# Kernel tuning notes

Hardware: AMD Instinct MI355X
Metric: run time of the kernel (lower is better)

The kernel has to match this reference:

```python
import jax, jax.numpy as jnp
import numpy as np

VAR0, VAR1 = 0.1, 0.2       # variances used by encode()
THRESH = 0.35               # overlap_thresh
NEGPOS = 7                  # negpos_ratio


def point_form(p):
    # (cx,cy,w,h) -> (xmin,ymin,xmax,ymax)
    return jnp.concatenate([p[:, :2] - p[:, 2:] / 2, p[:, :2] + p[:, 2:] / 2], axis=1)


def jaccard(a, b):
    # a:[G,4], b:[P,4] corner form -> IoU [G,P]
    lt = jnp.maximum(a[:, None, :2], b[None, :, :2])
    rb = jnp.minimum(a[:, None, 2:], b[None, :, 2:])
    wh = jnp.clip(rb - lt, 0.0, None)
    inter = wh[..., 0] * wh[..., 1]
    area_a = (a[:, 2] - a[:, 0]) * (a[:, 3] - a[:, 1])
    area_b = (b[:, 2] - b[:, 0]) * (b[:, 3] - b[:, 1])
    return inter / (area_a[:, None] + area_b[None, :] - inter)


def encode(matched, priors):
    g_cxcy = ((matched[:, :2] + matched[:, 2:]) / 2 - priors[:, :2]) / (VAR0 * priors[:, 2:])
    g_wh = jnp.log((matched[:, 2:] - matched[:, :2]) / priors[:, 2:]) / VAR1
    return jnp.concatenate([g_cxcy, g_wh], axis=1)


def encode_landm(matched, priors):
    m = matched.reshape(-1, 5, 2)                                  # [P,5,2]
    g = (m - priors[:, None, :2]) / (VAR0 * priors[:, None, 2:])
    return g.reshape(-1, 10)


def match_one(truths, labels, landms, priors, priors_pf):
    # truths:[G,4] labels:[G] landms:[G,10] priors:[P,4](cxcywh) priors_pf:[P,4](corner)
    G = truths.shape[0]
    P = priors.shape[0]
    ov = jaccard(truths, priors_pf)                                # [G,P]
    best_prior_ov = ov.max(axis=1)                                 # [G]
    best_prior_idx = ov.argmax(axis=1)                             # [G]
    valid_gt = best_prior_ov >= 0.2
    best_truth_ov = ov.max(axis=0)                                 # [P]
    best_truth_idx = ov.argmax(axis=0)                             # [P]
    # index_fill_(0, best_prior_idx[valid_gt], 2): 2 > any IoU, so max is equivalent
    forced_ov = jnp.zeros((P,), ov.dtype).at[best_prior_idx].max(jnp.where(valid_gt, 2.0, 0.0))
    best_truth_ov = jnp.maximum(best_truth_ov, forced_ov)
    forced_idx = jnp.full((P,), -1, jnp.int32).at[best_prior_idx].max(jnp.arange(G, dtype=jnp.int32))
    best_truth_idx = jnp.where(forced_idx >= 0, forced_idx, best_truth_idx.astype(jnp.int32))
    conf = labels[best_truth_idx].astype(jnp.int32)
    conf = jnp.where(best_truth_ov < THRESH, 0, conf)
    loc = encode(truths[best_truth_idx], priors)                   # [P,4]
    landm = encode_landm(landms[best_truth_idx], priors)           # [P,10]
    # if no valid gt, torch zeroes the targets for this sample
    any_valid = valid_gt.any()
    loc = jnp.where(any_valid, loc, 0.0)
    landm = jnp.where(any_valid, landm, 0.0)
    conf = jnp.where(any_valid, conf, 0)
    return loc, conf, landm


def smooth_l1(x):
    ax = jnp.abs(x)
    return jnp.where(ax < 1.0, 0.5 * ax * ax, ax - 0.5)


def setup_inputs() -> dict:
    key = jax.random.key(0)
    k1, k2, k3, k4, k5, k6, k7, k8, k9 = jax.random.split(key, 9)
    B, P, G, C = 64, 16800, 32, 2
    cls_data = jax.random.normal(k1, (B, P, C), jnp.float32)
    loc_data = jax.random.normal(k2, (B, P, 4), jnp.float32)
    landm_data = jax.random.normal(k3, (B, P, 10), jnp.float32)
    # priors in (cx,cy,w,h), w,h in [0.02,0.3]
    pc = jax.random.uniform(k4, (P, 2), jnp.float32)
    pwh = jax.random.uniform(k5, (P, 2), jnp.float32, 0.02, 0.3)
    priors = jnp.concatenate([pc, pwh], axis=1)
    # targets: [B,G,15] = 4 box (corner form, valid) + 10 landmarks + 1 label
    c = jax.random.uniform(k6, (B, G, 2), jnp.float32, 0.15, 0.85)
    s = jax.random.uniform(k7, (B, G, 2), jnp.float32, 0.02, 0.3)
    boxes = jnp.concatenate([c - s / 2, c + s / 2], axis=-1)
    lms = jax.random.uniform(k8, (B, G, 10), jnp.float32)
    labels = jnp.where(jax.random.uniform(k9, (B, G, 1)) < 0.3, -1.0, 1.0)
    targets = jnp.concatenate([boxes, lms, labels], axis=-1)
    return {"cls_data": cls_data, "loc_data": loc_data, "landm_data": landm_data,
            "priors": priors, "targets": targets}


def reference(cls_data, loc_data, landm_data, priors, targets):
    truths = targets[:, :, :4]
    landms = targets[:, :, 4:14]
    labels = targets[:, :, 14]
    priors_pf = point_form(priors)
    loc_t, conf_t, landm_t = jax.vmap(
        lambda t, l, lm: match_one(t, l, lm, priors, priors_pf))(truths, labels, landms)
    num, P = conf_t.shape

    # landmark loss (smooth L1 over conf_t > 0)
    pos1 = conf_t > 0
    N1 = jnp.maximum(pos1.sum().astype(jnp.float32), 1.0)
    loss_landm = jnp.sum(smooth_l1(landm_data - landm_t) * pos1[..., None].astype(landm_data.dtype))

    # localization loss (smooth L1 over conf_t != 0)
    pos = conf_t != 0
    conf_t = jnp.where(pos, 1, conf_t)                              # conf_t[pos] = 1
    loss_l = jnp.sum(smooth_l1(loc_data - loc_t) * pos[..., None].astype(loc_data.dtype))

    # hard negative mining on per-prior CE loss
    logz = jax.nn.logsumexp(cls_data, axis=-1)                      # [B,P]
    gold = jnp.take_along_axis(cls_data, conf_t[..., None], axis=-1)[..., 0]
    loss_c = jnp.where(pos, 0.0, logz - gold)
    loss_idx = jnp.argsort(-loss_c, axis=1)
    idx_rank = jnp.argsort(loss_idx, axis=1)
    num_pos = pos.sum(axis=1, keepdims=True)
    num_neg = jnp.clip(NEGPOS * num_pos, None, P - 1)
    neg = idx_rank < num_neg

    sel = (pos | neg).astype(cls_data.dtype)
    loss_conf = jnp.sum((logz - gold) * sel)

    N = jnp.maximum(num_pos.sum().astype(jnp.float32), 1.0)
    return loss_l / N, loss_conf / N, loss_landm / N1
```

## Files before the change

### kernel.cpp

```cpp
#include <hip/hip_runtime.h>
#include <hip/hip_bf16.h>
#include <math.h>


#define RCP(x) __builtin_amdgcn_rcpf(x)

constexpr int GN = 32;

__device__ __forceinline__ float sl1(float x) {
    float a = fabsf(x);
    return a < 1.f ? 0.5f * a * a : a - 0.5f;
}

constexpr int GPB = 4;
constexpr int GNT = 512;
__global__ __launch_bounds__(GNT)
void k_gt(const float4* __restrict__ priors, const float* __restrict__ targets,
          unsigned long long* __restrict__ keys, int P, int G) {
    const int b = blockIdx.y, g0 = blockIdx.x * GPB, tid = threadIdx.x;
    const int lane = tid & 63, w = tid >> 6;
    __shared__ float4 s_box[GPB];
    __shared__ float  s_at[GPB];
    __shared__ unsigned long long s_wk[GNT / 64][GPB];
    if (tid < GPB) {
        const float* t = targets + ((size_t)b * G + g0 + tid) * 15;
        float4 v = make_float4(t[0], t[1], t[2], t[3]);
        s_box[tid] = v;
        s_at[tid] = (v.z - v.x) * (v.w - v.y);
    }
    __syncthreads();
    float4 tb0 = s_box[0], tb1 = s_box[1], tb2 = s_box[2], tb3 = s_box[3];
    float at0 = s_at[0], at1 = s_at[1], at2 = s_at[2], at3 = s_at[3];

    float bv[GPB]; int bp[GPB];
    #pragma unroll
    for (int j = 0; j < GPB; ++j) { bv[j] = -1.f; bp[j] = 0; }

    for (int p = tid; p < P; p += GNT) {
        float4 pr = priors[p];
        float hx = pr.z * 0.5f, hy = pr.w * 0.5f;
        float px0 = pr.x - hx, py0 = pr.y - hy;
        float px1 = pr.x + hx, py1 = pr.y + hy;
        float ap = (px1 - px0) * (py1 - py0);
        #pragma unroll
        for (int j = 0; j < GPB; ++j) {
            float4 tb = j == 0 ? tb0 : (j == 1 ? tb1 : (j == 2 ? tb2 : tb3));
            float at = j == 0 ? at0 : (j == 1 ? at1 : (j == 2 ? at2 : at3));
            float lx = fmaxf(tb.x, px0), ly = fmaxf(tb.y, py0);
            float rx = fminf(tb.z, px1), ry = fminf(tb.w, py1);
            float iw = fmaxf(rx - lx, 0.f), ih = fmaxf(ry - ly, 0.f);
            float inter = iw * ih;
            float iou = inter * RCP(at + ap - inter);
            if (iou > bv[j]) { bv[j] = iou; bp[j] = p; }
        }
    }
    #pragma unroll
    for (int j = 0; j < GPB; ++j) {
        unsigned long long key =
            ((unsigned long long)__float_as_uint(bv[j]) << 32) | ~(unsigned)bp[j];
        #pragma unroll
        for (int o = 32; o > 0; o >>= 1) {
            unsigned long long t = __shfl_down(key, o, 64);
            if (t > key) key = t;
        }
        if (lane == 0) s_wk[w][j] = key;
    }
    __syncthreads();
    if (tid < GPB) {
        unsigned long long m = 0ull;
        #pragma unroll
        for (int q = 0; q < GNT / 64; ++q) { unsigned long long t = s_wk[q][tid]; if (t > m) m = t; }
        keys[b * G + g0 + tid] = m;
    }
}

__global__ __launch_bounds__(256)
void k_match(const float2* __restrict__ cls, const float4* __restrict__ loc,
             const float* __restrict__ lmd, const float4* __restrict__ priors,
             const float* __restrict__ targets,
             const unsigned long long* __restrict__ keys,
             float* __restrict__ bc, float* __restrict__ part, int P, int NB) {
    const int b = blockIdx.y, bx = blockIdx.x, tid = threadIdx.x;
    const int lane = tid & 63, w = tid >> 6;
    __shared__ float4 s_box[GN];
    __shared__ float  s_at[GN];
    __shared__ float  s_c035[GN];
    __shared__ float  s_lm[GN * 10];
    __shared__ float  s_lab[GN];
    __shared__ int    s_fg[256];
    __shared__ int    s_fv[256];
    __shared__ unsigned s_vm;
    __shared__ float  s_red[4][8];

    s_fg[tid] = -1; s_fv[tid] = 0;
    for (int i = tid; i < GN * 15; i += 256) {
        int g = i / 15, j = i - g * 15;
        float v = targets[((size_t)b * GN + g) * 15 + j];
        if (j < 4) ((float*)&s_box[g])[j] = v;
        else if (j < 14) s_lm[g * 10 + (j - 4)] = v;
        else s_lab[g] = v;
    }
    __syncthreads();
    if (tid < GN) {
        float4 v = s_box[tid];
        float at = (v.z - v.x) * (v.w - v.y);
        s_at[tid] = at;
        s_c035[tid] = 0.35f * at;
        unsigned long long key = keys[b * GN + tid];
        unsigned bp = ~(unsigned)key;
        bool val = __uint_as_float((unsigned)(key >> 32)) >= 0.2f;
        unsigned long long bal = __ballot(val);
        if (tid == 0) s_vm = (unsigned)bal;
        int local = (int)bp - bx * 256;
        if (local >= 0 && local < 256) {
            atomicMax(&s_fg[local], tid);
            if (val) atomicOr(&s_fv[local], 1);
        }
    }
    __syncthreads();
    const bool av = s_vm != 0u;
    const int  fidx = s_fg[tid];
    const bool fv = s_fv[tid] != 0;

    int p = bx * 256 + tid;
    const bool act = p < P;
    float4 pr = act ? priors[p] : make_float4(0.f, 0.f, 0.f, 0.f);
    float hx = pr.z * 0.5f, hy = pr.w * 0.5f;
    float px0 = pr.x - hx, py0 = pr.y - hy;
    float px1 = pr.x + hx, py1 = pr.y + hy;
    float ap = (px1 - px0) * (py1 - py0);
    if (!act) { px0 = py0 = INFINITY; px1 = py1 = -INFINITY; }

    float wx0 = px0, wy0 = py0, wx1 = px1, wy1 = py1;
    #pragma unroll
    for (int o = 32; o > 0; o >>= 1) {
        wx0 = fminf(wx0, __shfl_xor(wx0, o, 64));
        wy0 = fminf(wy0, __shfl_xor(wy0, o, 64));
        wx1 = fmaxf(wx1, __shfl_xor(wx1, o, 64));
        wy1 = fmaxf(wy1, __shfl_xor(wy1, o, 64));
    }
    bool sg = false;
    if (lane < GN) {
        float4 tb = s_box[lane];
        sg = (tb.x < wx1) && (tb.z > wx0) && (tb.y < wy1) && (tb.w > wy0);
    }
    unsigned mask = (unsigned)__ballot(sg);

    float qmax = -INFINITY;
    unsigned m2 = mask;
    while (m2) {
        int g = __ffs(m2) - 1; m2 &= m2 - 1;
        float4 tb = s_box[g];
        float lx = fmaxf(tb.x, px0), ly = fmaxf(tb.y, py0);
        float rx = fminf(tb.z, px1), ry = fminf(tb.w, py1);
        float iw = fmaxf(rx - lx, 0.f), ih = fmaxf(ry - ly, 0.f);
        float inter = iw * ih;
        qmax = fmaxf(qmax, fmaf(1.35f, inter, -s_c035[g]));
    }
    bool thr = act && (qmax >= 0.35f * ap);
    bool pos = act && av && (fv || thr);

    float lse = 0.f, d = 0.f;
    if (act) {
        float2 c = cls[(size_t)b * P + p];
        d = c.y - c.x;
        float m0 = fmaxf(d, 0.f);
        lse = m0 + __logf(__expf(-m0) + __expf(d - m0));
        bc[(size_t)b * P + p] = pos ? 0.f : lse;
    }

    float a_ll = 0.f, a_lm = 0.f, a_lcp = 0.f;
    bool posl = false;
    if (pos) {
        a_lcp = lse - d;
        int bti2 = fidx;
        if (fidx < 0) {
            float btv = -1.f;
            unsigned m3 = mask;
            while (m3) {
                int g = __ffs(m3) - 1; m3 &= m3 - 1;
                float4 tb = s_box[g];
                float lx = fmaxf(tb.x, px0), ly = fmaxf(tb.y, py0);
                float rx = fminf(tb.z, px1), ry = fminf(tb.w, py1);
                float iw = fmaxf(rx - lx, 0.f), ih = fmaxf(ry - ly, 0.f);
                float inter = iw * ih;
                float iou = inter * RCP(s_at[g] + ap - inter);
                if (iou > btv) { btv = iou; bti2 = g; }
            }
        }
        float4 tb = s_box[bti2];
        float rw = RCP(pr.z), rh = RCP(pr.w);
        float e0 = ((tb.x + tb.z) * 0.5f - pr.x) * rw * 10.f;
        float e1 = ((tb.y + tb.w) * 0.5f - pr.y) * rh * 10.f;
        float e2 = __logf((tb.z - tb.x) * rw) * 5.f;
        float e3 = __logf((tb.w - tb.y) * rh) * 5.f;
        float4 ld = loc[(size_t)b * P + p];
        a_ll = sl1(ld.x - e0) + sl1(ld.y - e1) + sl1(ld.z - e2) + sl1(ld.w - e3);
        if (s_lab[bti2] > 0.f) {
            posl = true;
            const float* lp = lmd + ((size_t)b * P + p) * 10;
            #pragma unroll
            for (int q = 0; q < 5; ++q) {
                float gx = (s_lm[bti2 * 10 + 2 * q]     - pr.x) * rw * 10.f;
                float gy = (s_lm[bti2 * 10 + 2 * q + 1] - pr.y) * rh * 10.f;
                a_lm += sl1(lp[2 * q] - gx) + sl1(lp[2 * q + 1] - gy);
            }
        }
    }

    unsigned long long bpos = __ballot(pos);
    int npw  = __popcll(bpos);
    int np1w = __popcll(__ballot(posl));
    if (bpos) {
        #pragma unroll
        for (int o = 32; o > 0; o >>= 1) {
            a_ll  += __shfl_down(a_ll,  o, 64);
            a_lm  += __shfl_down(a_lm,  o, 64);
            a_lcp += __shfl_down(a_lcp, o, 64);
        }
    }
    if (lane == 0) {
        s_red[w][0] = a_ll; s_red[w][1] = a_lm; s_red[w][2] = a_lcp;
        s_red[w][3] = (float)npw; s_red[w][4] = (float)np1w;
    }
    __syncthreads();
    if (tid == 0) {
        float* pp = part + ((size_t)b * NB + bx) * 8;
        #pragma unroll
        for (int j = 0; j < 5; ++j)
            pp[j] = s_red[0][j] + s_red[1][j] + s_red[2][j] + s_red[3][j];
    }
}

constexpr int SNT = 1024;
constexpr int SNI = 17;
__global__ __launch_bounds__(SNT)
void k_select(const float* __restrict__ bc, const float* __restrict__ part,
              float* __restrict__ part2, int P, int NB) {
    const int b = blockIdx.x, tid = threadIdx.x;
    const int lane = tid & 63, w = tid >> 6;
    unsigned ul[SNI];
    #pragma unroll
    for (int i = 0; i < SNI; ++i) {
        int idx = i * SNT + tid;
        ul[i] = idx < P ? __float_as_uint(bc[(size_t)b * P + idx]) : 0u;
    }
    __shared__ float s_r[5];
    if (w < 5) {
        float s = 0.f;
        for (int bx = lane; bx < NB; bx += 64) s += part[((size_t)b * NB + bx) * 8 + w];
        #pragma unroll
        for (int o = 32; o > 0; o >>= 1) s += __shfl_down(s, o, 64);
        if (lane == 0) s_r[w] = s;
    }
    __syncthreads();
    float t_ll = s_r[0], t_lm = s_r[1], t_lcp = s_r[2], t_np = s_r[3], t_np1 = s_r[4];
    int np = (int)(t_np + 0.5f);
    int k = np * 7;
    if (k > P - 1) k = P - 1;

    __shared__ int s_ri[16];
    __shared__ int s_i0;
    __shared__ float s_rf[16];
    float topk = 0.f;
    if (k > 0) {
        unsigned lo = 0u, hi = 0x7f800000u;
        while (lo < hi) {
            unsigned mid = lo + ((hi - lo + 1) >> 1);
            int cnt = 0;
            #pragma unroll
            for (int i = 0; i < SNI; ++i) cnt += (ul[i] >= mid) ? 1 : 0;
            #pragma unroll
            for (int o = 32; o > 0; o >>= 1) cnt += __shfl_down(cnt, o, 64);
            if (lane == 0) s_ri[w] = cnt;
            __syncthreads();
            if (tid == 0) {
                int r = 0;
                #pragma unroll
                for (int q = 0; q < 16; ++q) r += s_ri[q];
                s_i0 = r;
            }
            __syncthreads();
            if (s_i0 >= k) lo = mid; else hi = mid - 1;
        }
        float fT = __uint_as_float(lo);
        float s = 0.f; int c = 0;
        #pragma unroll
        for (int i = 0; i < SNI; ++i)
            if (ul[i] > lo) { s += __uint_as_float(ul[i]); c++; }
        #pragma unroll
        for (int o = 32; o > 0; o >>= 1) {
            s += __shfl_down(s, o, 64);
            c += __shfl_down(c, o, 64);
        }
        if (lane == 0) { s_rf[w] = s; s_ri[w] = c; }
        __syncthreads();
        if (tid == 0) {
            float ts = 0.f; int tc = 0;
            #pragma unroll
            for (int q = 0; q < 16; ++q) { ts += s_rf[q]; tc += s_ri[q]; }
            topk = ts + (float)(k - tc) * fT;
        }
    }
    if (tid == 0) {
        float* pp = part2 + b * 8;
        pp[0] = t_ll; pp[1] = t_lm; pp[2] = t_lcp;
        pp[3] = topk; pp[4] = t_np; pp[5] = t_np1;
    }
}

__global__ void k_final(const float* __restrict__ part2, float* __restrict__ out, int B) {
    int lane = threadIdx.x;
    float ll = 0, lm = 0, lcp = 0, tk = 0, np = 0, np1 = 0;
    for (int b = lane; b < B; b += 64) {
        const float* pp = part2 + b * 8;
        ll += pp[0]; lm += pp[1]; lcp += pp[2];
        tk += pp[3]; np += pp[4]; np1 += pp[5];
    }
    #pragma unroll
    for (int o = 32; o > 0; o >>= 1) {
        ll  += __shfl_down(ll, o, 64);
        lm  += __shfl_down(lm, o, 64);
        lcp += __shfl_down(lcp, o, 64);
        tk  += __shfl_down(tk, o, 64);
        np  += __shfl_down(np, o, 64);
        np1 += __shfl_down(np1, o, 64);
    }
    if (lane == 0) {
        float N = fmaxf(np, 1.f), N1 = fmaxf(np1, 1.f);
        out[0] = ll / N;
        out[1] = (lcp + tk) / N;
        out[2] = lm / N1;
    }
}

extern "C" void kernel_launch(void* const* d_in, const int* in_sizes, int n_in,
                              void* d_out, int out_size, void* d_ws, size_t ws_size,
                              hipStream_t stream) {
    const float2* cls    = (const float2*)d_in[0];
    const float4* loc    = (const float4*)d_in[1];
    const float* lmd     = (const float*)d_in[2];
    const float4* priors = (const float4*)d_in[3];
    const float* targets = (const float*)d_in[4];
    int P = in_sizes[3] / 4;
    int B = (in_sizes[1] / 4) / P;
    int NB = (P + 255) / 256;
    int G = in_sizes[4] / (15 * B);

    size_t off = 0;
    unsigned long long* keys = (unsigned long long*)d_ws; off += (size_t)B * G * 8;
    float* part  = (float*)((char*)d_ws + off); off += (size_t)B * NB * 8 * 4;
    float* part2 = (float*)((char*)d_ws + off); off += (size_t)B * 8 * 4;
    off = (off + 255) & ~(size_t)255;
    float* bc = (float*)((char*)d_ws + off);

    dim3 ggt((G + GPB - 1) / GPB, B);
    k_gt<<<ggt, GNT, 0, stream>>>(priors, targets, keys, P, G);
    dim3 gm(NB, B);
    k_match<<<gm, 256, 0, stream>>>(cls, loc, lmd, priors, targets, keys, bc, part, P, NB);
    k_select<<<B, SNT, 0, stream>>>(bc, part, part2, P, NB);
    k_final<<<1, 64, 0, stream>>>(part2, (float*)d_out, B);
}
```

Before: 96.60 us.

## Restructure match/select: bitmask positives, fuse CE into select, 4-way search, fused final

k_match now handles 1024 priors per block (4 per thread) with a fixed unrolled GT loop instead of wave-culled masks, and writes a positive bitmask in place of per-prior loss values. The logsumexp and CE computation moves into k_select, which reads cls directly and derives positive counts and loss sums there. The threshold search now tests three split points per round (quaternary search) to cut the number of barrier rounds. k_final is folded into k_select through a last-block atomic counter, removing one launch. In exchange, k_select does more per-batch serial work with fewer threads, each holding more values in registers.

```diff
diff --git a/kernel.cpp b/kernel.cpp
--- a/kernel.cpp
+++ b/kernel.cpp
@@ -4,6 +4,7 @@
 
 
 #define RCP(x) __builtin_amdgcn_rcpf(x)
+typedef unsigned long long u64;
 
 constexpr int GN = 32;
 
@@ -16,12 +17,13 @@
 constexpr int GNT = 512;
 __global__ __launch_bounds__(GNT)
 void k_gt(const float4* __restrict__ priors, const float* __restrict__ targets,
-          unsigned long long* __restrict__ keys, int P, int G) {
+          u64* __restrict__ keys, int* __restrict__ done, int P, int G) {
     const int b = blockIdx.y, g0 = blockIdx.x * GPB, tid = threadIdx.x;
     const int lane = tid & 63, w = tid >> 6;
+    if (blockIdx.x == 0 && blockIdx.y == 0 && tid == 0) *done = 0;
     __shared__ float4 s_box[GPB];
     __shared__ float  s_at[GPB];
-    __shared__ unsigned long long s_wk[GNT / 64][GPB];
+    __shared__ u64 s_wk[GNT / 64][GPB];
     if (tid < GPB) {
         const float* t = targets + ((size_t)b * G + g0 + tid) * 15;
         float4 v = make_float4(t[0], t[1], t[2], t[3]);
@@ -56,43 +58,44 @@
     }
     #pragma unroll
     for (int j = 0; j < GPB; ++j) {
-        unsigned long long key =
-            ((unsigned long long)__float_as_uint(bv[j]) << 32) | ~(unsigned)bp[j];
+        u64 key = ((u64)__float_as_uint(bv[j]) << 32) | ~(unsigned)bp[j];
         #pragma unroll
         for (int o = 32; o > 0; o >>= 1) {
-            unsigned long long t = __shfl_down(key, o, 64);
+            u64 t = __shfl_down(key, o, 64);
             if (t > key) key = t;
         }
         if (lane == 0) s_wk[w][j] = key;
     }
     __syncthreads();
     if (tid < GPB) {
-        unsigned long long m = 0ull;
-        #pragma unroll
-        for (int q = 0; q < GNT / 64; ++q) { unsigned long long t = s_wk[q][tid]; if (t > m) m = t; }
+        u64 m = 0ull;
+        #pragma unroll
+        for (int q = 0; q < GNT / 64; ++q) { u64 t = s_wk[q][tid]; if (t > m) m = t; }
         keys[b * G + g0 + tid] = m;
     }
 }
 
+constexpr int BPRI = 1024;
+constexpr int VPT  = 4;
+
 __global__ __launch_bounds__(256)
-void k_match(const float2* __restrict__ cls, const float4* __restrict__ loc,
-             const float* __restrict__ lmd, const float4* __restrict__ priors,
-             const float* __restrict__ targets,
-             const unsigned long long* __restrict__ keys,
-             float* __restrict__ bc, float* __restrict__ part, int P, int NB) {
+void k_match(const float4* __restrict__ loc, const float* __restrict__ lmd,
+             const float4* __restrict__ priors, const float* __restrict__ targets,
+             const u64* __restrict__ keys,
+             u64* __restrict__ pmask, float* __restrict__ part,
+             int P, int NBM, int MWA) {
     const int b = blockIdx.y, bx = blockIdx.x, tid = threadIdx.x;
     const int lane = tid & 63, w = tid >> 6;
     __shared__ float4 s_box[GN];
-    __shared__ float  s_at[GN];
-    __shared__ float  s_c035[GN];
+    __shared__ float  s_at[GN], s_c035[GN], s_lab[GN];
     __shared__ float  s_lm[GN * 10];
-    __shared__ float  s_lab[GN];
-    __shared__ int    s_fg[256];
-    __shared__ int    s_fv[256];
+    __shared__ int    s_fg[BPRI];
+    __shared__ unsigned s_fvb[BPRI / 32];
     __shared__ unsigned s_vm;
-    __shared__ float  s_red[4][8];
-
-    s_fg[tid] = -1; s_fv[tid] = 0;
+    __shared__ float  s_red[4][4];
+
+    for (int i = tid; i < BPRI; i += 256) s_fg[i] = -1;
+    if (tid < BPRI / 32) s_fvb[tid] = 0u;
     for (int i = tid; i < GN * 15; i += 256) {
         int g = i / 15, j = i - g * 15;
         float v = targets[((size_t)b * GN + g) * 15 + j];
@@ -106,231 +109,276 @@
         float at = (v.z - v.x) * (v.w - v.y);
         s_at[tid] = at;
         s_c035[tid] = 0.35f * at;
-        unsigned long long key = keys[b * GN + tid];
+        u64 key = keys[b * GN + tid];
         unsigned bp = ~(unsigned)key;
         bool val = __uint_as_float((unsigned)(key >> 32)) >= 0.2f;
-        unsigned long long bal = __ballot(val);
+        u64 bal = __ballot(val);
         if (tid == 0) s_vm = (unsigned)bal;
-        int local = (int)bp - bx * 256;
-        if (local >= 0 && local < 256) {
+        int local = (int)bp - bx * BPRI;
+        if (local >= 0 && local < BPRI) {
             atomicMax(&s_fg[local], tid);
-            if (val) atomicOr(&s_fv[local], 1);
+            if (val) atomicOr(&s_fvb[local >> 5], 1u << (local & 31));
         }
     }
     __syncthreads();
     const bool av = s_vm != 0u;
-    const int  fidx = s_fg[tid];
-    const bool fv = s_fv[tid] != 0;
-
-    int p = bx * 256 + tid;
-    const bool act = p < P;
-    float4 pr = act ? priors[p] : make_float4(0.f, 0.f, 0.f, 0.f);
-    float hx = pr.z * 0.5f, hy = pr.w * 0.5f;
-    float px0 = pr.x - hx, py0 = pr.y - hy;
-    float px1 = pr.x + hx, py1 = pr.y + hy;
-    float ap = (px1 - px0) * (py1 - py0);
-    if (!act) { px0 = py0 = INFINITY; px1 = py1 = -INFINITY; }
-
-    float wx0 = px0, wy0 = py0, wx1 = px1, wy1 = py1;
-    #pragma unroll
-    for (int o = 32; o > 0; o >>= 1) {
-        wx0 = fminf(wx0, __shfl_xor(wx0, o, 64));
-        wy0 = fminf(wy0, __shfl_xor(wy0, o, 64));
-        wx1 = fmaxf(wx1, __shfl_xor(wx1, o, 64));
-        wy1 = fmaxf(wy1, __shfl_xor(wy1, o, 64));
-    }
-    bool sg = false;
-    if (lane < GN) {
-        float4 tb = s_box[lane];
-        sg = (tb.x < wx1) && (tb.z > wx0) && (tb.y < wy1) && (tb.w > wy0);
-    }
-    unsigned mask = (unsigned)__ballot(sg);
-
-    float qmax = -INFINITY;
-    unsigned m2 = mask;
-    while (m2) {
-        int g = __ffs(m2) - 1; m2 &= m2 - 1;
+
+    float px0[VPT], py0[VPT], px1[VPT], py1[VPT], ap35[VPT], qmax[VPT];
+    #pragma unroll
+    for (int v = 0; v < VPT; ++v) {
+        int p = bx * BPRI + tid + 256 * v;
+        bool a = p < P;
+        float4 pr = a ? priors[p] : make_float4(0.f, 0.f, 0.f, 0.f);
+        float hx = pr.z * 0.5f, hy = pr.w * 0.5f;
+        px0[v] = pr.x - hx; py0[v] = pr.y - hy;
+        px1[v] = pr.x + hx; py1[v] = pr.y + hy;
+        ap35[v] = 0.35f * ((px1[v] - px0[v]) * (py1[v] - py0[v]));
+        qmax[v] = -INFINITY;
+    }
+    #pragma unroll
+    for (int g = 0; g < GN; ++g) {
         float4 tb = s_box[g];
-        float lx = fmaxf(tb.x, px0), ly = fmaxf(tb.y, py0);
-        float rx = fminf(tb.z, px1), ry = fminf(tb.w, py1);
-        float iw = fmaxf(rx - lx, 0.f), ih = fmaxf(ry - ly, 0.f);
-        float inter = iw * ih;
-        qmax = fmaxf(qmax, fmaf(1.35f, inter, -s_c035[g]));
-    }
-    bool thr = act && (qmax >= 0.35f * ap);
-    bool pos = act && av && (fv || thr);
-
-    float lse = 0.f, d = 0.f;
-    if (act) {
-        float2 c = cls[(size_t)b * P + p];
-        d = c.y - c.x;
-        float m0 = fmaxf(d, 0.f);
-        lse = m0 + __logf(__expf(-m0) + __expf(d - m0));
-        bc[(size_t)b * P + p] = pos ? 0.f : lse;
-    }
-
-    float a_ll = 0.f, a_lm = 0.f, a_lcp = 0.f;
-    bool posl = false;
-    if (pos) {
-        a_lcp = lse - d;
-        int bti2 = fidx;
-        if (fidx < 0) {
-            float btv = -1.f;
-            unsigned m3 = mask;
-            while (m3) {
-                int g = __ffs(m3) - 1; m3 &= m3 - 1;
-                float4 tb = s_box[g];
-                float lx = fmaxf(tb.x, px0), ly = fmaxf(tb.y, py0);
-                float rx = fminf(tb.z, px1), ry = fminf(tb.w, py1);
-                float iw = fmaxf(rx - lx, 0.f), ih = fmaxf(ry - ly, 0.f);
-                float inter = iw * ih;
-                float iou = inter * RCP(s_at[g] + ap - inter);
-                if (iou > btv) { btv = iou; bti2 = g; }
+        float c35 = s_c035[g];
+        #pragma unroll
+        for (int v = 0; v < VPT; ++v) {
+            float lx = fmaxf(tb.x, px0[v]), ly = fmaxf(tb.y, py0[v]);
+            float rx = fminf(tb.z, px1[v]), ry = fminf(tb.w, py1[v]);
+            float iw = fmaxf(rx - lx, 0.f), ih = fmaxf(ry - ly, 0.f);
+            qmax[v] = fmaxf(qmax[v], fmaf(1.35f, iw * ih, -c35));
+        }
+    }
+
+    float a_ll = 0.f, a_lm = 0.f, a_np1 = 0.f;
+    bool anyp = false;
+    #pragma unroll
+    for (int v = 0; v < VPT; ++v) {
+        int p = bx * BPRI + tid + 256 * v;
+        int local = tid + 256 * v;
+        bool a = p < P;
+        bool thr = a && (qmax[v] >= ap35[v]);
+        int fidx = s_fg[local];
+        bool fv = (s_fvb[local >> 5] >> (local & 31)) & 1u;
+        bool pos = a && av && (fv || thr);
+        anyp |= pos;
+        u64 bp = __ballot(pos);
+        if (lane == 0) pmask[(size_t)b * MWA + bx * (BPRI / 64) + v * 4 + w] = bp;
+        if (pos) {
+            float4 pr = priors[p];
+            int bti2 = fidx;
+            if (fidx < 0) {
+                float btv = -1.f;
+                float ap = (px1[v] - px0[v]) * (py1[v] - py0[v]);
+                #pragma unroll
+                for (int g = 0; g < GN; ++g) {
+                    float4 tb = s_box[g];
+                    float lx = fmaxf(tb.x, px0[v]), ly = fmaxf(tb.y, py0[v]);
+                    float rx = fminf(tb.z, px1[v]), ry = fminf(tb.w, py1[v]);
+                    float iw = fmaxf(rx - lx, 0.f), ih = fmaxf(ry - ly, 0.f);
+                    float inter = iw * ih;
+                    float iou = inter * RCP(s_at[g] + ap - inter);
+                    if (iou > btv) { btv = iou; bti2 = g; }
+                }
             }
-        }
-        float4 tb = s_box[bti2];
-        float rw = RCP(pr.z), rh = RCP(pr.w);
-        float e0 = ((tb.x + tb.z) * 0.5f - pr.x) * rw * 10.f;
-        float e1 = ((tb.y + tb.w) * 0.5f - pr.y) * rh * 10.f;
-        float e2 = __logf((tb.z - tb.x) * rw) * 5.f;
-        float e3 = __logf((tb.w - tb.y) * rh) * 5.f;
-        float4 ld = loc[(size_t)b * P + p];
-        a_ll = sl1(ld.x - e0) + sl1(ld.y - e1) + sl1(ld.z - e2) + sl1(ld.w - e3);
-        if (s_lab[bti2] > 0.f) {
-            posl = true;
-            const float* lp = lmd + ((size_t)b * P + p) * 10;
-            #pragma unroll
-            for (int q = 0; q < 5; ++q) {
-                float gx = (s_lm[bti2 * 10 + 2 * q]     - pr.x) * rw * 10.f;
-                float gy = (s_lm[bti2 * 10 + 2 * q + 1] - pr.y) * rh * 10.f;
-                a_lm += sl1(lp[2 * q] - gx) + sl1(lp[2 * q + 1] - gy);
+            float4 tb = s_box[bti2];
+            float rw = RCP(pr.z), rh = RCP(pr.w);
+            float e0 = ((tb.x + tb.z) * 0.5f - pr.x) * rw * 10.f;
+            float e1 = ((tb.y + tb.w) * 0.5f - pr.y) * rh * 10.f;
+            float e2 = __logf((tb.z - tb.x) * rw) * 5.f;
+            float e3 = __logf((tb.w - tb.y) * rh) * 5.f;
+            float4 ld = loc[(size_t)b * P + p];
+            a_ll += sl1(ld.x - e0) + sl1(ld.y - e1) + sl1(ld.z - e2) + sl1(ld.w - e3);
+            if (s_lab[bti2] > 0.f) {
+                a_np1 += 1.f;
+                const float* lp = lmd + ((size_t)b * P + p) * 10;
+                #pragma unroll
+                for (int q = 0; q < 5; ++q) {
+                    float gx = (s_lm[bti2 * 10 + 2 * q]     - pr.x) * rw * 10.f;
+                    float gy = (s_lm[bti2 * 10 + 2 * q + 1] - pr.y) * rh * 10.f;
+                    a_lm += sl1(lp[2 * q] - gx) + sl1(lp[2 * q + 1] - gy);
+                }
             }
         }
     }
-
-    unsigned long long bpos = __ballot(pos);
-    int npw  = __popcll(bpos);
-    int np1w = __popcll(__ballot(posl));
-    if (bpos) {
+    if (__ballot(anyp)) {
         #pragma unroll
         for (int o = 32; o > 0; o >>= 1) {
             a_ll  += __shfl_down(a_ll,  o, 64);
             a_lm  += __shfl_down(a_lm,  o, 64);
-            a_lcp += __shfl_down(a_lcp, o, 64);
-        }
-    }
-    if (lane == 0) {
-        s_red[w][0] = a_ll; s_red[w][1] = a_lm; s_red[w][2] = a_lcp;
-        s_red[w][3] = (float)npw; s_red[w][4] = (float)np1w;
-    }
+            a_np1 += __shfl_down(a_np1, o, 64);
+        }
+    }
+    if (lane == 0) { s_red[w][0] = a_ll; s_red[w][1] = a_lm; s_red[w][2] = a_np1; }
     __syncthreads();
     if (tid == 0) {
-        float* pp = part + ((size_t)b * NB + bx) * 8;
-        #pragma unroll
-        for (int j = 0; j < 5; ++j)
-            pp[j] = s_red[0][j] + s_red[1][j] + s_red[2][j] + s_red[3][j];
+        float* pp = part + ((size_t)b * NBM + bx) * 4;
+        pp[0] = s_red[0][0] + s_red[1][0] + s_red[2][0] + s_red[3][0];
+        pp[1] = s_red[0][1] + s_red[1][1] + s_red[2][1] + s_red[3][1];
+        pp[2] = s_red[0][2] + s_red[1][2] + s_red[2][2] + s_red[3][2];
     }
 }
 
-constexpr int SNT = 1024;
-constexpr int SNI = 17;
-__global__ __launch_bounds__(SNT)
-void k_select(const float* __restrict__ bc, const float* __restrict__ part,
-              float* __restrict__ part2, int P, int NB) {
+constexpr int KNT = 512;
+constexpr int KNI = 33;
+
+__global__ __launch_bounds__(KNT)
+void k_select(const float2* __restrict__ cls, const u64* __restrict__ pmask,
+              const float* __restrict__ part, float* __restrict__ part2,
+              float* __restrict__ out, int* __restrict__ done,
+              int P, int NBM, int MWA, int B) {
     const int b = blockIdx.x, tid = threadIdx.x;
     const int lane = tid & 63, w = tid >> 6;
-    unsigned ul[SNI];
-    #pragma unroll
-    for (int i = 0; i < SNI; ++i) {
-        int idx = i * SNT + tid;
-        ul[i] = idx < P ? __float_as_uint(bc[(size_t)b * P + idx]) : 0u;
-    }
-    __shared__ float s_r[5];
-    if (w < 5) {
-        float s = 0.f;
-        for (int bx = lane; bx < NB; bx += 64) s += part[((size_t)b * NB + bx) * 8 + w];
+    const int MW = (P + 63) >> 6;
+    __shared__ u64   s_mask[272];
+    __shared__ float s_pr3[3];
+    __shared__ float s_rf[8][2];
+    __shared__ u64   s_cw[8];
+    __shared__ u64   s_ct;
+    __shared__ int   s_k;
+    __shared__ float s_np, s_lcp;
+    __shared__ int   s_last;
+
+    if (tid < MW) s_mask[tid] = pmask[(size_t)b * MWA + tid];
+    else if (w >= 5 && w < 8) {
+        int j = w - 5;
+        float s = (lane < NBM) ? part[((size_t)b * NBM + lane) * 4 + j] : 0.f;
         #pragma unroll
         for (int o = 32; o > 0; o >>= 1) s += __shfl_down(s, o, 64);
-        if (lane == 0) s_r[w] = s;
-    }
-    __syncthreads();
-    float t_ll = s_r[0], t_lm = s_r[1], t_lcp = s_r[2], t_np = s_r[3], t_np1 = s_r[4];
-    int np = (int)(t_np + 0.5f);
-    int k = np * 7;
-    if (k > P - 1) k = P - 1;
-
-    __shared__ int s_ri[16];
-    __shared__ int s_i0;
-    __shared__ float s_rf[16];
+        if (lane == 0) s_pr3[j] = s;
+    }
+    __syncthreads();
+
+    float lcp = 0.f; int npc = 0;
+    unsigned ul[KNI];
+    #pragma unroll
+    for (int i = 0; i < KNI; ++i) {
+        int idx = i * KNT + tid;
+        unsigned u = 0u;
+        if (idx < P) {
+            float2 c = cls[(size_t)b * P + idx];
+            float d = c.y - c.x, m0 = fmaxf(d, 0.f);
+            float lse = m0 + __logf(__expf(-m0) + __expf(d - m0));
+            unsigned bit = (unsigned)(s_mask[idx >> 6] >> (idx & 63)) & 1u;
+            if (bit) { lcp += lse - d; npc++; }
+            else u = __float_as_uint(lse);
+        }
+        ul[i] = u;
+    }
+    float npf = (float)npc;
+    #pragma unroll
+    for (int o = 32; o > 0; o >>= 1) {
+        lcp += __shfl_down(lcp, o, 64);
+        npf += __shfl_down(npf, o, 64);
+    }
+    if (lane == 0) { s_rf[w][0] = lcp; s_rf[w][1] = npf; }
+    __syncthreads();
+    if (tid == 0) {
+        float lc = 0.f, np = 0.f;
+        #pragma unroll
+        for (int q = 0; q < 8; ++q) { lc += s_rf[q][0]; np += s_rf[q][1]; }
+        s_lcp = lc; s_np = np;
+        int k = (int)(np + 0.5f) * 7;
+        if (k > P - 1) k = P - 1;
+        s_k = k;
+    }
+    __syncthreads();
+    const int k = s_k;
+
     float topk = 0.f;
     if (k > 0) {
         unsigned lo = 0u, hi = 0x7f800000u;
         while (lo < hi) {
-            unsigned mid = lo + ((hi - lo + 1) >> 1);
-            int cnt = 0;
+            unsigned span = hi - lo;
+            unsigned m1 = lo + ((span + 3) >> 2);
+            unsigned m2 = lo + ((span + 1) >> 1);
+            unsigned m3 = hi - (span >> 2);
+            int c1 = 0, c2 = 0, c3 = 0;
             #pragma unroll
-            for (int i = 0; i < SNI; ++i) cnt += (ul[i] >= mid) ? 1 : 0;
+            for (int i = 0; i < KNI; ++i) {
+                unsigned u = ul[i];
+                c1 += u >= m1 ? 1 : 0;
+                c2 += u >= m2 ? 1 : 0;
+                c3 += u >= m3 ? 1 : 0;
+            }
+            u64 pk = (u64)c1 | ((u64)c2 << 20) | ((u64)c3 << 40);
             #pragma unroll
-            for (int o = 32; o > 0; o >>= 1) cnt += __shfl_down(cnt, o, 64);
-            if (lane == 0) s_ri[w] = cnt;
+            for (int o = 32; o > 0; o >>= 1) pk += __shfl_down(pk, o, 64);
+            if (lane == 0) s_cw[w] = pk;
             __syncthreads();
             if (tid == 0) {
-                int r = 0;
+                u64 t = 0;
                 #pragma unroll
-                for (int q = 0; q < 16; ++q) r += s_ri[q];
-                s_i0 = r;
+                for (int q = 0; q < 8; ++q) t += s_cw[q];
+                s_ct = t;
             }
             __syncthreads();
-            if (s_i0 >= k) lo = mid; else hi = mid - 1;
+            u64 t = s_ct;
+            int C1 = (int)(t & 0xFFFFFu);
+            int C2 = (int)((t >> 20) & 0xFFFFFu);
+            int C3 = (int)((t >> 40) & 0xFFFFFu);
+            if      (C3 >= k) lo = m3;
+            else if (C2 >= k) { lo = m2; hi = m3 - 1; }
+            else if (C1 >= k) { lo = m1; hi = m2 - 1; }
+            else hi = m1 - 1;
         }
         float fT = __uint_as_float(lo);
-        float s = 0.f; int c = 0;
-        #pragma unroll
-        for (int i = 0; i < SNI; ++i)
-            if (ul[i] > lo) { s += __uint_as_float(ul[i]); c++; }
+        float s = 0.f, cf = 0.f;
+        #pragma unroll
+        for (int i = 0; i < KNI; ++i)
+            if (ul[i] > lo) { s += __uint_as_float(ul[i]); cf += 1.f; }
         #pragma unroll
         for (int o = 32; o > 0; o >>= 1) {
-            s += __shfl_down(s, o, 64);
-            c += __shfl_down(c, o, 64);
-        }
-        if (lane == 0) { s_rf[w] = s; s_ri[w] = c; }
+            s  += __shfl_down(s, o, 64);
+            cf += __shfl_down(cf, o, 64);
+        }
+        if (lane == 0) { s_rf[w][0] = s; s_rf[w][1] = cf; }
         __syncthreads();
         if (tid == 0) {
-            float ts = 0.f; int tc = 0;
+            float ts = 0.f, tc = 0.f;
             #pragma unroll
-            for (int q = 0; q < 16; ++q) { ts += s_rf[q]; tc += s_ri[q]; }
-            topk = ts + (float)(k - tc) * fT;
+            for (int q = 0; q < 8; ++q) { ts += s_rf[q][0]; tc += s_rf[q][1]; }
+            topk = ts + ((float)k - tc) * fT;
         }
     }
     if (tid == 0) {
         float* pp = part2 + b * 8;
-        pp[0] = t_ll; pp[1] = t_lm; pp[2] = t_lcp;
-        pp[3] = topk; pp[4] = t_np; pp[5] = t_np1;
-    }
-}
-
-__global__ void k_final(const float* __restrict__ part2, float* __restrict__ out, int B) {
-    int lane = threadIdx.x;
-    float ll = 0, lm = 0, lcp = 0, tk = 0, np = 0, np1 = 0;
-    for (int b = lane; b < B; b += 64) {
-        const float* pp = part2 + b * 8;
-        ll += pp[0]; lm += pp[1]; lcp += pp[2];
-        tk += pp[3]; np += pp[4]; np1 += pp[5];
-    }
-    #pragma unroll
-    for (int o = 32; o > 0; o >>= 1) {
-        ll  += __shfl_down(ll, o, 64);
-        lm  += __shfl_down(lm, o, 64);
-        lcp += __shfl_down(lcp, o, 64);
-        tk  += __shfl_down(tk, o, 64);
-        np  += __shfl_down(np, o, 64);
-        np1 += __shfl_down(np1, o, 64);
-    }
-    if (lane == 0) {
-        float N = fmaxf(np, 1.f), N1 = fmaxf(np1, 1.f);
-        out[0] = ll / N;
-        out[1] = (lcp + tk) / N;
-        out[2] = lm / N1;
+        pp[0] = s_pr3[0];
+        pp[1] = s_pr3[1];
+        pp[2] = s_lcp;
+        pp[3] = topk;
+        pp[4] = s_np;
+        pp[5] = s_pr3[2];
+        __threadfence();
+        int old = atomicAdd(done, 1);
+        s_last = (old == B - 1) ? 1 : 0;
+    }
+    __syncthreads();
+    if (s_last && w == 0) {
+        __threadfence();
+        volatile float* vp = part2;
+        float ll = 0.f, lm = 0.f, lc = 0.f, tk = 0.f, np = 0.f, np1 = 0.f;
+        for (int bb = lane; bb < B; bb += 64) {
+            ll  += vp[bb * 8 + 0];
+            lm  += vp[bb * 8 + 1];
+            lc  += vp[bb * 8 + 2];
+            tk  += vp[bb * 8 + 3];
+            np  += vp[bb * 8 + 4];
+            np1 += vp[bb * 8 + 5];
+        }
+        #pragma unroll
+        for (int o = 32; o > 0; o >>= 1) {
+            ll  += __shfl_down(ll,  o, 64);
+            lm  += __shfl_down(lm,  o, 64);
+            lc  += __shfl_down(lc,  o, 64);
+            tk  += __shfl_down(tk,  o, 64);
+            np  += __shfl_down(np,  o, 64);
+            np1 += __shfl_down(np1, o, 64);
+        }
+        if (lane == 0) {
+            float N = fmaxf(np, 1.f), N1 = fmaxf(np1, 1.f);
+            out[0] = ll / N;
+            out[1] = (lc + tk) / N;
+            out[2] = lm / N1;
+        }
     }
 }
 
@@ -344,20 +392,22 @@
     const float* targets = (const float*)d_in[4];
     int P = in_sizes[3] / 4;
     int B = (in_sizes[1] / 4) / P;
-    int NB = (P + 255) / 256;
     int G = in_sizes[4] / (15 * B);
+    int NBM = (P + BPRI - 1) / BPRI;
+    int MWA = NBM * (BPRI / 64);
 
     size_t off = 0;
-    unsigned long long* keys = (unsigned long long*)d_ws; off += (size_t)B * G * 8;
-    float* part  = (float*)((char*)d_ws + off); off += (size_t)B * NB * 8 * 4;
-    float* part2 = (float*)((char*)d_ws + off); off += (size_t)B * 8 * 4;
-    off = (off + 255) & ~(size_t)255;
-    float* bc = (float*)((char*)d_ws + off);
+    u64* keys  = (u64*)d_ws;                         off += (size_t)B * G * 8;
+    u64* pmask = (u64*)((char*)d_ws + off);          off += (size_t)B * MWA * 8;
+    float* part  = (float*)((char*)d_ws + off);      off += (size_t)B * NBM * 4 * 4;
+    float* part2 = (float*)((char*)d_ws + off);      off += (size_t)B * 8 * 4;
+    int* done = (int*)((char*)d_ws + off);           off += 256;
 
     dim3 ggt((G + GPB - 1) / GPB, B);
-    k_gt<<<ggt, GNT, 0, stream>>>(priors, targets, keys, P, G);
-    dim3 gm(NB, B);
-    k_match<<<gm, 256, 0, stream>>>(cls, loc, lmd, priors, targets, keys, bc, part, P, NB);
-    k_select<<<B, SNT, 0, stream>>>(bc, part, part2, P, NB);
-    k_final<<<1, 64, 0, stream>>>(part2, (float*)d_out, B);
+    k_gt<<<ggt, GNT, 0, stream>>>(priors, targets, keys, done, P, G);
+    dim3 gm(NBM, B);
+    k_match<<<gm, 256, 0, stream>>>(loc, lmd, priors, targets, keys, pmask, part,
+                                    P, NBM, MWA);
+    k_select<<<B, KNT, 0, stream>>>(cls, pmask, part, part2, (float*)d_out, done,
+                                    P, NBM, MWA, B);
 }
```

After: 119.9 us. +24.1%, slower.

## Fuse final reduction into select, use 4-way threshold search, drop match culling

Applied to the files above, without the earlier changes.

Several changes at once. The final-reduction kernel is folded into k_select through a last-block atomic counter, which removes one launch. The binary threshold search becomes a quaternary search with packed 64-bit counts, roughly halving the iterations and their block barriers. k_match drops the wave-bounding-box culling and instead runs a fully unrolled loop over all 32 GT boxes. k_gt doubles its block size. The risks are extra IoU work wherever culling used to prune boxes, and the correctness of the done-counter protocol.

```diff
diff --git a/kernel.cpp b/kernel.cpp
--- a/kernel.cpp
+++ b/kernel.cpp
@@ -4,6 +4,7 @@
 
 
 #define RCP(x) __builtin_amdgcn_rcpf(x)
+typedef unsigned long long u64;
 
 constexpr int GN = 32;
 
@@ -13,15 +14,16 @@
 }
 
 constexpr int GPB = 4;
-constexpr int GNT = 512;
+constexpr int GNT = 1024;
 __global__ __launch_bounds__(GNT)
 void k_gt(const float4* __restrict__ priors, const float* __restrict__ targets,
-          unsigned long long* __restrict__ keys, int P, int G) {
+          u64* __restrict__ keys, int* __restrict__ done, int P, int G) {
     const int b = blockIdx.y, g0 = blockIdx.x * GPB, tid = threadIdx.x;
     const int lane = tid & 63, w = tid >> 6;
+    if (blockIdx.x == 0 && blockIdx.y == 0 && tid == 0) *done = 0;
     __shared__ float4 s_box[GPB];
     __shared__ float  s_at[GPB];
-    __shared__ unsigned long long s_wk[GNT / 64][GPB];
+    __shared__ u64 s_wk[GNT / 64][GPB];
     if (tid < GPB) {
         const float* t = targets + ((size_t)b * G + g0 + tid) * 15;
         float4 v = make_float4(t[0], t[1], t[2], t[3]);
@@ -56,20 +58,19 @@
     }
     #pragma unroll
     for (int j = 0; j < GPB; ++j) {
-        unsigned long long key =
-            ((unsigned long long)__float_as_uint(bv[j]) << 32) | ~(unsigned)bp[j];
+        u64 key = ((u64)__float_as_uint(bv[j]) << 32) | ~(unsigned)bp[j];
         #pragma unroll
         for (int o = 32; o > 0; o >>= 1) {
-            unsigned long long t = __shfl_down(key, o, 64);
+            u64 t = __shfl_down(key, o, 64);
             if (t > key) key = t;
         }
         if (lane == 0) s_wk[w][j] = key;
     }
     __syncthreads();
     if (tid < GPB) {
-        unsigned long long m = 0ull;
-        #pragma unroll
-        for (int q = 0; q < GNT / 64; ++q) { unsigned long long t = s_wk[q][tid]; if (t > m) m = t; }
+        u64 m = 0ull;
+        #pragma unroll
+        for (int q = 0; q < GNT / 64; ++q) { u64 t = s_wk[q][tid]; if (t > m) m = t; }
         keys[b * G + g0 + tid] = m;
     }
 }
@@ -77,16 +78,13 @@
 __global__ __launch_bounds__(256)
 void k_match(const float2* __restrict__ cls, const float4* __restrict__ loc,
              const float* __restrict__ lmd, const float4* __restrict__ priors,
-             const float* __restrict__ targets,
-             const unsigned long long* __restrict__ keys,
+             const float* __restrict__ targets, const u64* __restrict__ keys,
              float* __restrict__ bc, float* __restrict__ part, int P, int NB) {
     const int b = blockIdx.y, bx = blockIdx.x, tid = threadIdx.x;
     const int lane = tid & 63, w = tid >> 6;
     __shared__ float4 s_box[GN];
-    __shared__ float  s_at[GN];
-    __shared__ float  s_c035[GN];
+    __shared__ float  s_at[GN], s_c035[GN], s_lab[GN];
     __shared__ float  s_lm[GN * 10];
-    __shared__ float  s_lab[GN];
     __shared__ int    s_fg[256];
     __shared__ int    s_fv[256];
     __shared__ unsigned s_vm;
@@ -106,10 +104,10 @@
         float at = (v.z - v.x) * (v.w - v.y);
         s_at[tid] = at;
         s_c035[tid] = 0.35f * at;
-        unsigned long long key = keys[b * GN + tid];
+        u64 key = keys[b * GN + tid];
         unsigned bp = ~(unsigned)key;
         bool val = __uint_as_float((unsigned)(key >> 32)) >= 0.2f;
-        unsigned long long bal = __ballot(val);
+        u64 bal = __ballot(val);
         if (tid == 0) s_vm = (unsigned)bal;
         int local = (int)bp - bx * 256;
         if (local >= 0 && local < 256) {
@@ -119,8 +117,6 @@
     }
     __syncthreads();
     const bool av = s_vm != 0u;
-    const int  fidx = s_fg[tid];
-    const bool fv = s_fv[tid] != 0;
 
     int p = bx * 256 + tid;
     const bool act = p < P;
@@ -129,35 +125,20 @@
     float px0 = pr.x - hx, py0 = pr.y - hy;
     float px1 = pr.x + hx, py1 = pr.y + hy;
     float ap = (px1 - px0) * (py1 - py0);
-    if (!act) { px0 = py0 = INFINITY; px1 = py1 = -INFINITY; }
-
-    float wx0 = px0, wy0 = py0, wx1 = px1, wy1 = py1;
+    float ap35 = 0.35f * ap;
+
+    float qmax = -INFINITY;
     #pragma unroll
-    for (int o = 32; o > 0; o >>= 1) {
-        wx0 = fminf(wx0, __shfl_xor(wx0, o, 64));
-        wy0 = fminf(wy0, __shfl_xor(wy0, o, 64));
-        wx1 = fmaxf(wx1, __shfl_xor(wx1, o, 64));
-        wy1 = fmaxf(wy1, __shfl_xor(wy1, o, 64));
-    }
-    bool sg = false;
-    if (lane < GN) {
-        float4 tb = s_box[lane];
-        sg = (tb.x < wx1) && (tb.z > wx0) && (tb.y < wy1) && (tb.w > wy0);
-    }
-    unsigned mask = (unsigned)__ballot(sg);
-
-    float qmax = -INFINITY;
-    unsigned m2 = mask;
-    while (m2) {
-        int g = __ffs(m2) - 1; m2 &= m2 - 1;
+    for (int g = 0; g < GN; ++g) {
         float4 tb = s_box[g];
         float lx = fmaxf(tb.x, px0), ly = fmaxf(tb.y, py0);
         float rx = fminf(tb.z, px1), ry = fminf(tb.w, py1);
         float iw = fmaxf(rx - lx, 0.f), ih = fmaxf(ry - ly, 0.f);
-        float inter = iw * ih;
-        qmax = fmaxf(qmax, fmaf(1.35f, inter, -s_c035[g]));
-    }
-    bool thr = act && (qmax >= 0.35f * ap);
+        qmax = fmaxf(qmax, fmaf(1.35f, iw * ih, -s_c035[g]));
+    }
+    bool thr = act && (qmax >= ap35);
+    int fidx = s_fg[tid];
+    bool fv = s_fv[tid] != 0;
     bool pos = act && av && (fv || thr);
 
     float lse = 0.f, d = 0.f;
@@ -176,9 +157,8 @@
         int bti2 = fidx;
         if (fidx < 0) {
             float btv = -1.f;
-            unsigned m3 = mask;
-            while (m3) {
-                int g = __ffs(m3) - 1; m3 &= m3 - 1;
+            #pragma unroll 1
+            for (int g = 0; g < GN; ++g) {
                 float4 tb = s_box[g];
                 float lx = fmaxf(tb.x, px0), ly = fmaxf(tb.y, py0);
                 float rx = fminf(tb.z, px1), ry = fminf(tb.w, py1);
@@ -208,7 +188,7 @@
         }
     }
 
-    unsigned long long bpos = __ballot(pos);
+    u64 bpos = __ballot(pos);
     int npw  = __popcll(bpos);
     int np1w = __popcll(__ballot(posl));
     if (bpos) {
@@ -232,20 +212,26 @@
     }
 }
 
-constexpr int SNT = 1024;
-constexpr int SNI = 17;
-__global__ __launch_bounds__(SNT)
+constexpr int KNT = 1024;
+constexpr int KNI = 17;
+__global__ __launch_bounds__(KNT)
 void k_select(const float* __restrict__ bc, const float* __restrict__ part,
-              float* __restrict__ part2, int P, int NB) {
+              float* __restrict__ part2, float* __restrict__ out,
+              int* __restrict__ done, int P, int NB, int B) {
     const int b = blockIdx.x, tid = threadIdx.x;
     const int lane = tid & 63, w = tid >> 6;
-    unsigned ul[SNI];
+    __shared__ float s_r[5];
+    __shared__ u64   s_cw[16];
+    __shared__ u64   s_ct;
+    __shared__ float s_rf[16][2];
+    __shared__ int   s_last;
+
+    unsigned ul[KNI];
     #pragma unroll
-    for (int i = 0; i < SNI; ++i) {
-        int idx = i * SNT + tid;
+    for (int i = 0; i < KNI; ++i) {
+        int idx = i * KNT + tid;
         ul[i] = idx < P ? __float_as_uint(bc[(size_t)b * P + idx]) : 0u;
     }
-    __shared__ float s_r[5];
     if (w < 5) {
         float s = 0.f;
         for (int bx = lane; bx < NB; bx += 64) s += part[((size_t)b * NB + bx) * 8 + w];
@@ -254,83 +240,103 @@
         if (lane == 0) s_r[w] = s;
     }
     __syncthreads();
-    float t_ll = s_r[0], t_lm = s_r[1], t_lcp = s_r[2], t_np = s_r[3], t_np1 = s_r[4];
-    int np = (int)(t_np + 0.5f);
-    int k = np * 7;
+    const float t_ll = s_r[0], t_lm = s_r[1], t_lcp = s_r[2];
+    const float t_np = s_r[3], t_np1 = s_r[4];
+    int k = (int)(t_np + 0.5f) * 7;
     if (k > P - 1) k = P - 1;
 
-    __shared__ int s_ri[16];
-    __shared__ int s_i0;
-    __shared__ float s_rf[16];
     float topk = 0.f;
     if (k > 0) {
         unsigned lo = 0u, hi = 0x7f800000u;
         while (lo < hi) {
-            unsigned mid = lo + ((hi - lo + 1) >> 1);
-            int cnt = 0;
+            unsigned span = hi - lo;
+            unsigned m1 = lo + ((span + 3) >> 2);
+            unsigned m2 = lo + ((span + 1) >> 1);
+            unsigned m3 = hi - (span >> 2);
+            int c1 = 0, c2 = 0, c3 = 0;
             #pragma unroll
-            for (int i = 0; i < SNI; ++i) cnt += (ul[i] >= mid) ? 1 : 0;
+            for (int i = 0; i < KNI; ++i) {
+                unsigned u = ul[i];
+                c1 += u >= m1 ? 1 : 0;
+                c2 += u >= m2 ? 1 : 0;
+                c3 += u >= m3 ? 1 : 0;
+            }
+            u64 pk = (u64)c1 | ((u64)c2 << 20) | ((u64)c3 << 40);
             #pragma unroll
-            for (int o = 32; o > 0; o >>= 1) cnt += __shfl_down(cnt, o, 64);
-            if (lane == 0) s_ri[w] = cnt;
+            for (int o = 32; o > 0; o >>= 1) pk += __shfl_down(pk, o, 64);
+            if (lane == 0) s_cw[w] = pk;
             __syncthreads();
             if (tid == 0) {
-                int r = 0;
+                u64 t = 0;
                 #pragma unroll
-                for (int q = 0; q < 16; ++q) r += s_ri[q];
-                s_i0 = r;
+                for (int q = 0; q < 16; ++q) t += s_cw[q];
+                s_ct = t;
             }
             __syncthreads();
-            if (s_i0 >= k) lo = mid; else hi = mid - 1;
+            u64 t = s_ct;
+            int C1 = (int)(t & 0xFFFFFu);
+            int C2 = (int)((t >> 20) & 0xFFFFFu);
+            int C3 = (int)((t >> 40) & 0xFFFFFu);
+            if      (C3 >= k) lo = m3;
+            else if (C2 >= k) { lo = m2; hi = m3 - 1; }
+            else if (C1 >= k) { lo = m1; hi = m2 - 1; }
+            else hi = m1 - 1;
         }
         float fT = __uint_as_float(lo);
-        float s = 0.f; int c = 0;
-        #pragma unroll
-        for (int i = 0; i < SNI; ++i)
-            if (ul[i] > lo) { s += __uint_as_float(ul[i]); c++; }
+        float s = 0.f, cf = 0.f;
+        #pragma unroll
+        for (int i = 0; i < KNI; ++i)
+            if (ul[i] > lo) { s += __uint_as_float(ul[i]); cf += 1.f; }
         #pragma unroll
         for (int o = 32; o > 0; o >>= 1) {
-            s += __shfl_down(s, o, 64);
-            c += __shfl_down(c, o, 64);
-        }
-        if (lane == 0) { s_rf[w] = s; s_ri[w] = c; }
+            s  += __shfl_down(s, o, 64);
+            cf += __shfl_down(cf, o, 64);
+        }
+        if (lane == 0) { s_rf[w][0] = s; s_rf[w][1] = cf; }
         __syncthreads();
         if (tid == 0) {
-            float ts = 0.f; int tc = 0;
+            float ts = 0.f, tc = 0.f;
             #pragma unroll
-            for (int q = 0; q < 16; ++q) { ts += s_rf[q]; tc += s_ri[q]; }
-            topk = ts + (float)(k - tc) * fT;
+            for (int q = 0; q < 16; ++q) { ts += s_rf[q][0]; tc += s_rf[q][1]; }
+            topk = ts + ((float)k - tc) * fT;
         }
     }
     if (tid == 0) {
         float* pp = part2 + b * 8;
         pp[0] = t_ll; pp[1] = t_lm; pp[2] = t_lcp;
         pp[3] = topk; pp[4] = t_np; pp[5] = t_np1;
-    }
-}
-
-__global__ void k_final(const float* __restrict__ part2, float* __restrict__ out, int B) {
-    int lane = threadIdx.x;
-    float ll = 0, lm = 0, lcp = 0, tk = 0, np = 0, np1 = 0;
-    for (int b = lane; b < B; b += 64) {
-        const float* pp = part2 + b * 8;
-        ll += pp[0]; lm += pp[1]; lcp += pp[2];
-        tk += pp[3]; np += pp[4]; np1 += pp[5];
-    }
-    #pragma unroll
-    for (int o = 32; o > 0; o >>= 1) {
-        ll  += __shfl_down(ll, o, 64);
-        lm  += __shfl_down(lm, o, 64);
-        lcp += __shfl_down(lcp, o, 64);
-        tk  += __shfl_down(tk, o, 64);
-        np  += __shfl_down(np, o, 64);
-        np1 += __shfl_down(np1, o, 64);
-    }
-    if (lane == 0) {
-        float N = fmaxf(np, 1.f), N1 = fmaxf(np1, 1.f);
-        out[0] = ll / N;
-        out[1] = (lcp + tk) / N;
-        out[2] = lm / N1;
+        __threadfence();
+        int old = atomicAdd(done, 1);
+        s_last = (old == B - 1) ? 1 : 0;
+    }
+    __syncthreads();
+    if (s_last && w == 0) {
+        __threadfence();
+        volatile float* vp = part2;
+        float ll = 0.f, lm = 0.f, lc = 0.f, tk = 0.f, np = 0.f, np1 = 0.f;
+        for (int bb = lane; bb < B; bb += 64) {
+            ll  += vp[bb * 8 + 0];
+            lm  += vp[bb * 8 + 1];
+            lc  += vp[bb * 8 + 2];
+            tk  += vp[bb * 8 + 3];
+            np  += vp[bb * 8 + 4];
+            np1 += vp[bb * 8 + 5];
+        }
+        #pragma unroll
+        for (int o = 32; o > 0; o >>= 1) {
+            ll  += __shfl_down(ll,  o, 64);
+            lm  += __shfl_down(lm,  o, 64);
+            lc  += __shfl_down(lc,  o, 64);
+            tk  += __shfl_down(tk,  o, 64);
+            np  += __shfl_down(np,  o, 64);
+            np1 += __shfl_down(np1, o, 64);
+        }
+        if (lane == 0) {
+            float N = fmaxf(np, 1.f), N1 = fmaxf(np1, 1.f);
+            out[0] = ll / N;
+            out[1] = (lc + tk) / N;
+            out[2] = lm / N1;
+        }
     }
 }
 
@@ -344,20 +350,20 @@
     const float* targets = (const float*)d_in[4];
     int P = in_sizes[3] / 4;
     int B = (in_sizes[1] / 4) / P;
+    int G = in_sizes[4] / (15 * B);
     int NB = (P + 255) / 256;
-    int G = in_sizes[4] / (15 * B);
 
     size_t off = 0;
-    unsigned long long* keys = (unsigned long long*)d_ws; off += (size_t)B * G * 8;
-    float* part  = (float*)((char*)d_ws + off); off += (size_t)B * NB * 8 * 4;
-    float* part2 = (float*)((char*)d_ws + off); off += (size_t)B * 8 * 4;
+    u64* keys    = (u64*)d_ws;                     off += (size_t)B * G * 8;
+    float* part  = (float*)((char*)d_ws + off);    off += (size_t)B * NB * 8 * 4;
+    float* part2 = (float*)((char*)d_ws + off);    off += (size_t)B * 8 * 4;
+    int* done    = (int*)((char*)d_ws + off);      off += 256;
     off = (off + 255) & ~(size_t)255;
-    float* bc = (float*)((char*)d_ws + off);
+    float* bc    = (float*)((char*)d_ws + off);
 
     dim3 ggt((G + GPB - 1) / GPB, B);
-    k_gt<<<ggt, GNT, 0, stream>>>(priors, targets, keys, P, G);
+    k_gt<<<ggt, GNT, 0, stream>>>(priors, targets, keys, done, P, G);
     dim3 gm(NB, B);
     k_match<<<gm, 256, 0, stream>>>(cls, loc, lmd, priors, targets, keys, bc, part, P, NB);
-    k_select<<<B, SNT, 0, stream>>>(bc, part, part2, P, NB);
-    k_final<<<1, 64, 0, stream>>>(part2, (float*)d_out, B);
-}
+    k_select<<<B, KNT, 0, stream>>>(bc, part, part2, (float*)d_out, done, P, NB, B);
+}
```

Result: faster. 93.51 us (-3.2%).
